# Kernel tuning notes

Hardware: AMD Instinct MI355X
Metric: run time of the kernel (lower is better)

Reference implementation:

```python
import jax, jax.numpy as jnp
import numpy as np

DIM, DEPTH, HEADS = 1024, 6, 16
B, N = 2, 1024
QB = 128.0   # 8-bit activation absmax quant: Qb = 2**(8-1)
EPS = 1e-5


def setup_inputs() -> dict:
    key = jax.random.key(0)
    ks = jax.random.split(key, 4)
    x = jax.random.normal(ks[0], (B, N, DIM), dtype=jnp.float32)
    # BitLinear weights (per layer, two per FFN block), latent fp weights
    ff_w1 = jax.random.normal(ks[1], (DEPTH, DIM, DIM), dtype=jnp.float32) * 0.02
    ff_w2 = jax.random.normal(ks[2], (DEPTH, DIM, DIM), dtype=jnp.float32) * 0.02
    # LayerNorm params (inside FeedForward) and final norm
    ff_ln_g = jnp.ones((DEPTH, DIM), jnp.float32)
    ff_ln_b = jnp.zeros((DEPTH, DIM), jnp.float32)
    final_ln_g = jnp.ones((DIM,), jnp.float32)
    final_ln_b = jnp.zeros((DIM,), jnp.float32)
    return dict(x=x, ff_ln_g=ff_ln_g, ff_ln_b=ff_ln_b, ff_w1=ff_w1,
                ff_w2=ff_w2, final_ln_g=final_ln_g, final_ln_b=final_ln_b)


def layernorm(x, g, b):
    m = jnp.mean(x, axis=-1, keepdims=True)
    v = jnp.mean((x - m) ** 2, axis=-1, keepdims=True)
    return (x - m) * jax.lax.rsqrt(v + EPS) * g + b


def bitlinear(x, w):
    # BitNet b1: binarize weights around their mean, absmax-quantize activations to 8 bits,
    # int-style matmul, then rescale by beta*gamma/Qb.
    alpha = jnp.mean(w)
    w_b = jnp.sign(w - alpha)                 # ternary/binary weights {-1,0,+1}
    beta = jnp.mean(jnp.abs(w))               # ||W||_1 / (n*m)
    gamma = jnp.max(jnp.abs(x))               # activation absmax
    x_q = jnp.clip(x * (QB / gamma), -QB + EPS, QB - EPS)
    y = jnp.einsum('...i,oi->...o', x_q, w_b)
    return y * (beta * gamma / QB)


def attend(x):
    # non-flash multi-head self-attention, q=k=v=x (Attend has no projections)
    b, n, d = x.shape
    dh = d // HEADS
    q = x.reshape(b, n, HEADS, dh).transpose(0, 2, 1, 3)          # bhnd
    scores = jnp.einsum('bhid,bhjd->bhij', q, q) * (dh ** -0.5)   # [B,H,N,N]
    attn = jax.nn.softmax(scores, axis=-1)
    out = jnp.einsum('bhij,bhjd->bhid', attn, q)
    return out.transpose(0, 2, 1, 3).reshape(b, n, d)


def reference(x, ff_ln_g, ff_ln_b, ff_w1, ff_w2, final_ln_g, final_ln_b):
    for i in range(DEPTH):
        x = attend(x) + x
        h = layernorm(x, ff_ln_g[i], ff_ln_b[i])
        h = bitlinear(h, ff_w1[i])
        h = jax.nn.gelu(h, approximate=False)   # torch nn.GELU default = exact
        h = bitlinear(h, ff_w2[i])
        x = h + x
    return layernorm(x, final_ln_g, final_ln_b)
```

## Files before the change

### kernel.cpp

```cpp
#include <hip/hip_runtime.h>
#include <math.h>

typedef __attribute__((ext_vector_type(4))) float f32x4;
typedef __attribute__((ext_vector_type(8))) _Float16 f16x8;

__device__ __forceinline__ f32x4 mfma16h(f16x8 a, f16x8 b, f32x4 c){
  return __builtin_amdgcn_mfma_f32_16x16x32_f16(a, b, c, 0, 0, 0);
}
__device__ __forceinline__ void gload_lds16(const void* g, void* l){
  __builtin_amdgcn_global_load_lds((const __attribute__((address_space(1))) void*)g,
                                   (__attribute__((address_space(3))) void*)l, 16, 0, 0);
}

#define EXPC 0.1803368801111204f

__global__ __launch_bounds__(256) void k_wstats(const float* __restrict__ w1, const float* __restrict__ w2,
                                                double* __restrict__ dsum, double* __restrict__ dabs){
  const int mat = blockIdx.y;
  const float* wp = (mat < 6) ? (w1 + (size_t)mat*1048576) : (w2 + (size_t)(mat-6)*1048576);
  const f32x4* wv = (const f32x4*)wp + (size_t)blockIdx.x*8192;
  double s = 0.0, a = 0.0;
  for (int j = 0; j < 32; j++){
    f32x4 v = wv[j*256 + threadIdx.x];
    s += (double)v.x + (double)v.y + (double)v.z + (double)v.w;
    a += (double)fabsf(v.x) + (double)fabsf(v.y) + (double)fabsf(v.z) + (double)fabsf(v.w);
  }
  for (int d = 1; d < 64; d <<= 1){ s += __shfl_xor(s, d); a += __shfl_xor(a, d); }
  __shared__ double red[8];
  const int w = threadIdx.x >> 6;
  if ((threadIdx.x & 63) == 0){ red[w*2] = s; red[w*2+1] = a; }
  __syncthreads();
  if (threadIdx.x == 0){
    double S = red[0]+red[2]+red[4]+red[6], A = red[1]+red[3]+red[5]+red[7];
    atomicAdd(&dsum[mat], S);
    atomicAdd(&dabs[mat], A);
  }
}

__global__ __launch_bounds__(256) void k_binarize(const float* __restrict__ w1, const float* __restrict__ w2,
                                                  const double* __restrict__ dsum, _Float16* __restrict__ wb){
  const int blk = blockIdx.x;
  const int mat = blk >> 9;
  const float alpha = (float)(dsum[mat] * (1.0/1048576.0));
  const float* wp = (mat < 6) ? (w1 + (size_t)mat*1048576) : (w2 + (size_t)(mat-6)*1048576);
  const size_t off = (size_t)(blk & 511)*2048 + (size_t)threadIdx.x*8;
  const int n = (int)(off >> 10), k = (int)(off & 1023);
  f32x4 v0 = *(const f32x4*)(wp + off), v1 = *(const f32x4*)(wp + off + 4);
  float vv[8] = {v0.x,v0.y,v0.z,v0.w,v1.x,v1.y,v1.z,v1.w};
  f16x8 pk;
  #pragma unroll
  for (int e = 0; e < 8; e++){
    float d = vv[e] - alpha;
    pk[e] = d > 0.f ? (_Float16)1.0f : (d < 0.f ? (_Float16)(-1.0f) : (_Float16)0.0f);
  }
  const size_t addr = (size_t)mat*1048576 + (size_t)n*1024 + (size_t)((k & ~63) + ((k & 63) ^ ((n&7)*8)));
  *(f16x8*)&wb[addr] = pk;
}

__global__ __launch_bounds__(256) void k_presplit(const float* __restrict__ x,
                                                  _Float16* __restrict__ Kh, _Float16* __restrict__ Kl,
                                                  _Float16* __restrict__ Vh, _Float16* __restrict__ Vl){
  __shared__ _Float16 lh[64*72], ll[64*72];
  const int t = blockIdx.x, bh = blockIdx.y, b = bh>>4, h = bh&15;
  const int n = threadIdx.x>>2, c0 = (threadIdx.x&3)*16;
  const float* src = x + (size_t)b*1048576 + (size_t)(t*64+n)*1024 + h*64 + c0;
  const size_t kbase = ((size_t)bh*1024 + t*64 + n)*64;
  const int sw = (n&7)*8;
  #pragma unroll
  for (int j = 0; j < 2; j++){
    f32x4 v0 = *(const f32x4*)(src + j*8);
    f32x4 v1 = *(const f32x4*)(src + j*8 + 4);
    float vv[8] = {v0.x,v0.y,v0.z,v0.w,v1.x,v1.y,v1.z,v1.w};
    f16x8 Hv, Lv;
    #pragma unroll
    for (int e = 0; e < 8; e++){
      _Float16 hh = (_Float16)vv[e];
      Hv[e] = hh; Lv[e] = (_Float16)(vv[e] - (float)hh);
      const int d = c0 + j*8 + e;
      lh[d*72 + n] = Hv[e]; ll[d*72 + n] = Lv[e];
    }
    const int db = c0 + j*8;
    *(f16x8*)&Kh[kbase + (db ^ sw)] = Hv;
    *(f16x8*)&Kl[kbase + (db ^ sw)] = Lv;
  }
  __syncthreads();
  const int d = threadIdx.x>>2, n0c = (threadIdx.x&3)*16;
  const size_t vbase = ((size_t)bh*64 + d)*1024 + t*64;
  const int sw2 = (d&7)*8;
  #pragma unroll
  for (int j = 0; j < 2; j++){
    f16x8 Hv, Lv;
    #pragma unroll
    for (int e = 0; e < 8; e++){
      Hv[e] = lh[d*72 + n0c + j*8 + e];
      Lv[e] = ll[d*72 + n0c + j*8 + e];
    }
    const int nb = n0c + j*8;
    *(f16x8*)&Vh[vbase + (nb ^ sw2)] = Hv;
    *(f16x8*)&Vl[vbase + (nb ^ sw2)] = Lv;
  }
}

__global__ __launch_bounds__(256) void k_attn(const _Float16* __restrict__ Kh, const _Float16* __restrict__ Kl,
                                              const _Float16* __restrict__ Vh, const _Float16* __restrict__ Vl,
                                              const float* __restrict__ xin, float* __restrict__ xout){
  __shared__ _Float16 smb[40960];
  _Float16* ps_h = smb + 32768;
  _Float16* ps_l = smb + 36864;
  const int tid = threadIdx.x, w = tid>>6, l = tid&63, g = l>>4, r16 = l&15;
  const int bh = blockIdx.x, qt = blockIdx.y, b = bh>>4, h = bh&15;
  const int swr = (r16&7)*8;
  const _Float16* Kbh = Kh + (size_t)bh*65536;
  const _Float16* Kbl = Kl + (size_t)bh*65536;

  #define ASTAGE(buf, t) { _Float16* Bp = smb + (buf)*16384;                                    \
    _Pragma("unroll")                                                                            \
    for (int j = 0; j < 2; j++){                                                                 \
      const int cb = (j*4 + w)*64; const int c = cb + l;                                         \
      gload_lds16(Kbh + (size_t)(t)*4096 + (size_t)c*8, Bp + cb*8);                              \
      gload_lds16(Kbl + (size_t)(t)*4096 + (size_t)c*8, Bp + 4096 + cb*8);                       \
      gload_lds16(Vh + ((size_t)bh*64 + (c>>3))*1024 + (t)*64 + (c&7)*8, Bp + 8192 + cb*8);      \
      gload_lds16(Vl + ((size_t)bh*64 + (c>>3))*1024 + (t)*64 + (c&7)*8, Bp + 12288 + cb*8);     \
    } }

  const _Float16* Qsh = Kbh + (size_t)qt*4096;
  const _Float16* Qsl = Kbl + (size_t)qt*4096;
  #pragma unroll
  for (int j = 0; j < 2; j++){
    const int cb = (j*4 + w)*64;
    gload_lds16(Qsh + (size_t)(cb + l)*8, ps_h + cb*8);
    gload_lds16(Qsl + (size_t)(cb + l)*8, ps_l + cb*8);
  }
  ASTAGE(0, 0);
  __syncthreads();
  const int qrow = w*16 + r16;
  const f16x8 aqh0 = *(const f16x8*)&ps_h[qrow*64 + ((g*8) ^ swr)];
  const f16x8 aqh1 = *(const f16x8*)&ps_h[qrow*64 + ((32 + g*8) ^ swr)];
  const f16x8 aql0 = *(const f16x8*)&ps_l[qrow*64 + ((g*8) ^ swr)];
  const f16x8 aql1 = *(const f16x8*)&ps_l[qrow*64 + ((32 + g*8) ^ swr)];
  __syncthreads();
  float mI[4], lI[4]; f32x4 acc[4];
  #pragma unroll
  for (int i = 0; i < 4; i++){ mI[i] = -1e30f; lI[i] = 0.f; acc[i] = (f32x4){0.f,0.f,0.f,0.f}; }

  for (int t = 0; t < 16; t++){
    if (t < 15) ASTAGE((t+1)&1, t+1);
    const _Float16* kt_h = smb + (t&1)*16384;
    const _Float16* kt_l = kt_h + 4096;
    const _Float16* vt_h = kt_h + 8192;
    const _Float16* vt_l = kt_h + 12288;
    f32x4 s[4];
    #pragma unroll
    for (int c = 0; c < 4; c++){
      const int rk = c*16 + r16;
      const f16x8 kh0 = *(const f16x8*)&kt_h[rk*64 + ((g*8) ^ swr)];
      const f16x8 kh1 = *(const f16x8*)&kt_h[rk*64 + ((32+g*8) ^ swr)];
      const f16x8 kl0 = *(const f16x8*)&kt_l[rk*64 + ((g*8) ^ swr)];
      const f16x8 kl1 = *(const f16x8*)&kt_l[rk*64 + ((32+g*8) ^ swr)];
      f32x4 z = (f32x4){0.f,0.f,0.f,0.f};
      z = mfma16h(aqh0, kh0, z);
      z = mfma16h(aqh1, kh1, z);
      z = mfma16h(aql0, kh0, z);
      z = mfma16h(aql1, kh1, z);
      z = mfma16h(aqh0, kl0, z);
      z = mfma16h(aqh1, kl1, z);
      s[c] = z;
    }
    float rmax[4], rsum[4], mnC[4];
    #pragma unroll
    for (int i = 0; i < 4; i++) rmax[i] = fmaxf(fmaxf(s[0][i],s[1][i]), fmaxf(s[2][i],s[3][i]));
    for (int d = 1; d < 16; d <<= 1)
      #pragma unroll
      for (int i = 0; i < 4; i++) rmax[i] = fmaxf(rmax[i], __shfl_xor(rmax[i], d));
    const float dmax = fmaxf(fmaxf(rmax[0]-mI[0], rmax[1]-mI[1]), fmaxf(rmax[2]-mI[2], rmax[3]-mI[3]));
    if (dmax > 44.36f){
      #pragma unroll
      for (int i = 0; i < 4; i++){
        const float mn = fmaxf(mI[i], rmax[i]);
        const float fac = exp2f((mI[i] - mn)*EXPC);
        lI[i] *= fac;
        mI[i] = mn;
        #pragma unroll
        for (int dc = 0; dc < 4; dc++) acc[dc][i] *= fac;
      }
    }
    #pragma unroll
    for (int i = 0; i < 4; i++){ mnC[i] = mI[i]*EXPC; rsum[i] = 0.f; }
    #pragma unroll
    for (int c = 0; c < 4; c++)
      #pragma unroll
      for (int i = 0; i < 4; i++){
        float p = exp2f(fmaf(s[c][i], EXPC, -mnC[i]));
        _Float16 ph = (_Float16)p;
        const int prow = w*16 + g*4 + i;
        const int pcol = (c*16 + r16) ^ ((2*g + (i>>1))*8);
        ps_h[prow*64 + pcol] = ph;
        ps_l[prow*64 + pcol] = (_Float16)(p - (float)ph);
        rsum[i] += p;
      }
    for (int d = 1; d < 16; d <<= 1)
      #pragma unroll
      for (int i = 0; i < 4; i++) rsum[i] += __shfl_xor(rsum[i], d);
    #pragma unroll
    for (int i = 0; i < 4; i++) lI[i] += rsum[i];
    const int psw = (r16>>1)*8;
    #pragma unroll
    for (int ks = 0; ks < 2; ks++){
      const f16x8 aph = *(const f16x8*)&ps_h[(w*16+r16)*64 + ((ks*32 + g*8) ^ psw)];
      const f16x8 apl = *(const f16x8*)&ps_l[(w*16+r16)*64 + ((ks*32 + g*8) ^ psw)];
      #pragma unroll
      for (int dc = 0; dc < 4; dc++){
        const int vr = dc*16 + r16;
        const f16x8 bvh = *(const f16x8*)&vt_h[vr*64 + ((ks*32 + g*8) ^ swr)];
        const f16x8 bvl = *(const f16x8*)&vt_l[vr*64 + ((ks*32 + g*8) ^ swr)];
        acc[dc] = mfma16h(aph, bvh, acc[dc]);
        acc[dc] = mfma16h(apl, bvh, acc[dc]);
        acc[dc] = mfma16h(aph, bvl, acc[dc]);
      }
    }
    __syncthreads();
  }
  #undef ASTAGE
  #pragma unroll
  for (int dc = 0; dc < 4; dc++)
    #pragma unroll
    for (int i = 0; i < 4; i++){
      const int row = qt*64 + w*16 + g*4 + i;
      const size_t idx = (size_t)b*1048576 + (size_t)row*1024 + h*64 + dc*16 + r16;
      xout[idx] = acc[dc][i]/lI[i] + xin[idx];
    }
}

template<int SPLIT>
__global__ __launch_bounds__(256) void k_ln(const float* __restrict__ x, const float* __restrict__ gg,
                                            const float* __restrict__ bb, float* __restrict__ outf,
                                            _Float16* __restrict__ Oh, _Float16* __restrict__ Ol){
  const int row = blockIdx.x*4 + (threadIdx.x>>6);
  const int lane = threadIdx.x & 63;
  const float* xr = x + (size_t)row*1024;
  f32x4 v[4];
  float s = 0.f, q = 0.f;
  #pragma unroll
  for (int c = 0; c < 2; c++){
    v[c*2]   = *(const f32x4*)(xr + c*512 + lane*8);
    v[c*2+1] = *(const f32x4*)(xr + c*512 + lane*8 + 4);
    #pragma unroll
    for (int e = 0; e < 4; e++){
      s += v[c*2][e] + v[c*2+1][e];
      q += v[c*2][e]*v[c*2][e] + v[c*2+1][e]*v[c*2+1][e];
    }
  }
  for (int d = 1; d < 64; d <<= 1){ s += __shfl_xor(s,d); q += __shfl_xor(q,d); }
  const float mean = s * (1.f/1024.f);
  const float var  = q * (1.f/1024.f) - mean*mean;
  const float rstd = rsqrtf(var + 1e-5f);
  #pragma unroll
  for (int c = 0; c < 2; c++){
    const int col = c*512 + lane*8;
    f32x4 g0 = *(const f32x4*)(gg + col), g1 = *(const f32x4*)(gg + col + 4);
    f32x4 b0 = *(const f32x4*)(bb + col), b1 = *(const f32x4*)(bb + col + 4);
    float h[8];
    #pragma unroll
    for (int e = 0; e < 4; e++){
      h[e]   = (v[c*2][e]  -mean)*rstd*g0[e] + b0[e];
      h[e+4] = (v[c*2+1][e]-mean)*rstd*g1[e] + b1[e];
    }
    if (SPLIT){
      f16x8 Hv, Lv;
      #pragma unroll
      for (int e = 0; e < 8; e++){
        _Float16 hh = (_Float16)h[e];
        Hv[e] = hh; Lv[e] = (_Float16)(h[e] - (float)hh);
      }
      const size_t addr = (size_t)row*1024 + c*512 + (lane>>3)*64 + (((lane&7)*8) ^ ((row&7)*8));
      *(f16x8*)&Oh[addr] = Hv;
      *(f16x8*)&Ol[addr] = Lv;
    } else {
      f32x4 o0, o1;
      #pragma unroll
      for (int e = 0; e < 4; e++){ o0[e] = h[e]; o1[e] = h[e+4]; }
      *(f32x4*)(outf + (size_t)row*1024 + col) = o0;
      *(f32x4*)(outf + (size_t)row*1024 + col + 4) = o1;
    }
  }
}

template<int MODE>
__global__ __launch_bounds__(256) void k_gemm(const _Float16* __restrict__ Ah, const _Float16* __restrict__ Al,
                                              const _Float16* __restrict__ Wg,
                                              float* __restrict__ out32,
                                              _Float16* __restrict__ Oh, _Float16* __restrict__ Ol,
                                              const double* __restrict__ dabs_slot){
  __shared__ _Float16 smb[24576];
  const int tid = threadIdx.x, w = tid>>6, l = tid&63, g = l>>4, r16 = l&15;
  const int wm = w>>1, wn = w&1;
  const int n0 = blockIdx.x*64, m0 = blockIdx.y*64;
  const float scale = (float)(*dabs_slot * (1.0/1048576.0));
  const int swr = (r16&7)*8;
  f32x4 acc[2][2] = {};
  #define STAGE(buf, k0) { _Float16* Bp = smb + (buf)*12288;                              \
    _Pragma("unroll")                                                                     \
    for (int j = 0; j < 2; j++){                                                          \
      const int cb = (j*4 + w)*64; const int c = cb + l;                                  \
      const int r = c>>3; const int cc = (c&7)*8;                                         \
      gload_lds16(Ah + (size_t)(m0 + r)*1024 + (k0) + cc, Bp + cb*8);                     \
      gload_lds16(Al + (size_t)(m0 + r)*1024 + (k0) + cc, Bp + 4096 + cb*8);              \
      gload_lds16(Wg + (size_t)(n0 + r)*1024 + (k0) + cc, Bp + 8192 + cb*8);              \
    } }
  STAGE(0, 0);
  __syncthreads();
  for (int t = 0; t < 16; t++){
    if (t < 15) STAGE((t+1)&1, (t+1)*64);
    const _Float16* Bp = smb + (t&1)*12288;
    #pragma unroll
    for (int kk = 0; kk < 2; kk++){
      f16x8 ah[2], al[2], bf[2];
      const int col = (kk*32 + g*8) ^ swr;
      #pragma unroll
      for (int mi = 0; mi < 2; mi++){
        const int row = wm*32 + mi*16 + r16;
        ah[mi] = *(const f16x8*)&Bp[row*64 + col];
        al[mi] = *(const f16x8*)&Bp[4096 + row*64 + col];
      }
      #pragma unroll
      for (int ni = 0; ni < 2; ni++){
        const int row = wn*32 + ni*16 + r16;
        bf[ni] = *(const f16x8*)&Bp[8192 + row*64 + col];
      }
      #pragma unroll
      for (int mi = 0; mi < 2; mi++)
        #pragma unroll
        for (int ni = 0; ni < 2; ni++){
          acc[mi][ni] = mfma16h(ah[mi], bf[ni], acc[mi][ni]);
          acc[mi][ni] = mfma16h(al[mi], bf[ni], acc[mi][ni]);
        }
    }
    __syncthreads();
  }
  #undef STAGE
  #pragma unroll
  for (int mi = 0; mi < 2; mi++)
    #pragma unroll
    for (int ni = 0; ni < 2; ni++)
      #pragma unroll
      for (int i = 0; i < 4; i++){
        const int rr = m0 + wm*32 + mi*16 + g*4 + i;
        const int cc = n0 + wn*32 + ni*16 + r16;
        float vv = acc[mi][ni][i] * scale;
        if (MODE == 0){
          vv = 0.5f*vv*(1.f + erff(vv*0.70710678118f));
          _Float16 hh = (_Float16)vv;
          const size_t addr = (size_t)rr*1024 + (cc & ~63) + ((cc & 63) ^ ((rr&7)*8));
          Oh[addr] = hh;
          Ol[addr] = (_Float16)(vv - (float)hh);
        } else {
          out32[(size_t)rr*1024 + cc] += vv;
        }
      }
}

extern "C" void kernel_launch(void* const* d_in, const int* in_sizes, int n_in,
                              void* d_out, int out_size, void* d_ws, size_t ws_size,
                              hipStream_t stream){
  const float* x_in = (const float*)d_in[0];
  const float* ln_g = (const float*)d_in[1];
  const float* ln_b = (const float*)d_in[2];
  const float* w1   = (const float*)d_in[3];
  const float* w2   = (const float*)d_in[4];
  const float* fg   = (const float*)d_in[5];
  const float* fb   = (const float*)d_in[6];

  char* ws = (char*)d_ws;
  double*   dsum  = (double*)ws;
  double*   dabs  = (double*)(ws + 96);
  _Float16* wb = (_Float16*)(ws + 256);
  size_t o = 256 + 12ull*1048576ull*2ull;
  float* xA = (float*)(ws + o); o += 2048ull*1024*4;
  float* xB = (float*)(ws + o); o += 2048ull*1024*4;
  _Float16* Kh = (_Float16*)(ws + o); o += 2048ull*1024*2;
  _Float16* Kl = (_Float16*)(ws + o); o += 2048ull*1024*2;
  _Float16* Vh = (_Float16*)(ws + o); o += 2048ull*1024*2;
  _Float16* Vl = (_Float16*)(ws + o); o += 2048ull*1024*2;
  _Float16* Ahb = (_Float16*)(ws + o); o += 2048ull*1024*2;
  _Float16* Alb = (_Float16*)(ws + o); o += 2048ull*1024*2;
  _Float16* Ghb = (_Float16*)(ws + o); o += 2048ull*1024*2;
  _Float16* Glb = (_Float16*)(ws + o); o += 2048ull*1024*2;

  hipMemsetAsync(ws, 0, 256, stream);
  k_wstats  <<<dim3(32,12), 256, 0, stream>>>(w1, w2, dsum, dabs);
  k_binarize<<<6144,        256, 0, stream>>>(w1, w2, dsum, wb);

  const float* xc = x_in;
  for (int i = 0; i < 6; i++){
    float* xn = (i & 1) ? xB : xA;
    k_presplit<<<dim3(16,32), 256, 0, stream>>>(xc, Kh, Kl, Vh, Vl);
    k_attn    <<<dim3(32,16), 256, 0, stream>>>(Kh, Kl, Vh, Vl, xc, xn);
    k_ln<1>   <<<512, 256, 0, stream>>>(xn, ln_g + (size_t)i*1024, ln_b + (size_t)i*1024,
                                        nullptr, Ahb, Alb);
    k_gemm<0> <<<dim3(16,32), 256, 0, stream>>>(Ahb, Alb, wb + (size_t)i*1048576,
                                                nullptr, Ghb, Glb, &dabs[i]);
    k_gemm<1> <<<dim3(16,32), 256, 0, stream>>>(Ghb, Glb, wb + (size_t)(6+i)*1048576,
                                                xn, nullptr, nullptr, &dabs[6+i]);
    xc = xn;
  }
  k_ln<0><<<512, 256, 0, stream>>>(xc, fg, fb, (float*)d_out, nullptr, nullptr);
}
```

Before: 596.3 us.

## Compute transposed S tile so P stays in registers, skipping LDS round-trip

Swaps the MFMA operands in the QK^T step so each lane holds one query row's scores across the key dimension. The P fragments can then be packed directly into registers as the A-operand of the PV MFMA, instead of being written to and read back from LDS. The K and Q swizzle and permutation are reworked to match the new fragment layout. Row max and sum reductions shrink to two cross-lane shuffles on a single scalar per lane, and the epilogue uses a reciprocal multiply. The new index permutations are intricate and a mistake would silently break correctness.

```diff
diff --git a/kernel.cpp b/kernel.cpp
--- a/kernel.cpp
+++ b/kernel.cpp
@@ -65,7 +65,7 @@
   const int n = threadIdx.x>>2, c0 = (threadIdx.x&3)*16;
   const float* src = x + (size_t)b*1048576 + (size_t)(t*64+n)*1024 + h*64 + c0;
   const size_t kbase = ((size_t)bh*1024 + t*64 + n)*64;
-  const int sw = (n&7)*8;
+  const int sw = ((((n>>4)&1)<<2) | (((n>>3)&1)<<1) | (n&1)) * 8;
   #pragma unroll
   for (int j = 0; j < 2; j++){
     f32x4 v0 = *(const f32x4*)(src + j*8);
@@ -105,43 +105,55 @@
                                               const _Float16* __restrict__ Vh, const _Float16* __restrict__ Vl,
                                               const float* __restrict__ xin, float* __restrict__ xout){
   __shared__ _Float16 smb[40960];
-  _Float16* ps_h = smb + 32768;
-  _Float16* ps_l = smb + 36864;
+  _Float16* qs_h = smb + 32768;
+  _Float16* qs_l = smb + 36864;
   const int tid = threadIdx.x, w = tid>>6, l = tid&63, g = l>>4, r16 = l&15;
   const int bh = blockIdx.x, qt = blockIdx.y, b = bh>>4, h = bh&15;
-  const int swr = (r16&7)*8;
   const _Float16* Kbh = Kh + (size_t)bh*65536;
   const _Float16* Kbl = Kl + (size_t)bh*65536;
 
-  #define ASTAGE(buf, t) { _Float16* Bp = smb + (buf)*16384;                                    \
-    _Pragma("unroll")                                                                            \
-    for (int j = 0; j < 2; j++){                                                                 \
-      const int cb = (j*4 + w)*64; const int c = cb + l;                                         \
-      gload_lds16(Kbh + (size_t)(t)*4096 + (size_t)c*8, Bp + cb*8);                              \
-      gload_lds16(Kbl + (size_t)(t)*4096 + (size_t)c*8, Bp + 4096 + cb*8);                       \
-      gload_lds16(Vh + ((size_t)bh*64 + (c>>3))*1024 + (t)*64 + (c&7)*8, Bp + 8192 + cb*8);      \
-      gload_lds16(Vl + ((size_t)bh*64 + (c>>3))*1024 + (t)*64 + (c&7)*8, Bp + 12288 + cb*8);     \
+  size_t koffK[2], voff[2];
+  int cbj[2];
+  #pragma unroll
+  for (int j = 0; j < 2; j++){
+    const int cb = (j*4 + w)*64, c = cb + l;
+    const int p  = c>>3;
+    const int kp = (p&32) | ((p&12)<<1) | ((p&16)>>2) | (p&3);
+    cbj[j]   = cb;
+    koffK[j] = (size_t)kp*64 + (size_t)(l&7)*8;
+    voff[j]  = ((size_t)bh*64 + (c>>3))*1024 + (size_t)(c&7)*8;
+  }
+  #define ASTAGE(buf, t) { _Float16* Bp = smb + (buf)*16384;                         \
+    _Pragma("unroll")                                                                 \
+    for (int j = 0; j < 2; j++){                                                      \
+      gload_lds16(Kbh + (size_t)(t)*4096 + koffK[j], Bp + cbj[j]*8);                  \
+      gload_lds16(Kbl + (size_t)(t)*4096 + koffK[j], Bp + 4096 + cbj[j]*8);           \
+      gload_lds16(Vh + voff[j] + (t)*64, Bp + 8192 + cbj[j]*8);                       \
+      gload_lds16(Vl + voff[j] + (t)*64, Bp + 12288 + cbj[j]*8);                      \
     } }
 
   const _Float16* Qsh = Kbh + (size_t)qt*4096;
   const _Float16* Qsl = Kbl + (size_t)qt*4096;
   #pragma unroll
   for (int j = 0; j < 2; j++){
-    const int cb = (j*4 + w)*64;
-    gload_lds16(Qsh + (size_t)(cb + l)*8, ps_h + cb*8);
-    gload_lds16(Qsl + (size_t)(cb + l)*8, ps_l + cb*8);
+    const int cb = cbj[j];
+    gload_lds16(Qsh + (size_t)(cb + l)*8, qs_h + cb*8);
+    gload_lds16(Qsl + (size_t)(cb + l)*8, qs_l + cb*8);
   }
   ASTAGE(0, 0);
   __syncthreads();
   const int qrow = w*16 + r16;
-  const f16x8 aqh0 = *(const f16x8*)&ps_h[qrow*64 + ((g*8) ^ swr)];
-  const f16x8 aqh1 = *(const f16x8*)&ps_h[qrow*64 + ((32 + g*8) ^ swr)];
-  const f16x8 aql0 = *(const f16x8*)&ps_l[qrow*64 + ((g*8) ^ swr)];
-  const f16x8 aql1 = *(const f16x8*)&ps_l[qrow*64 + ((32 + g*8) ^ swr)];
-  __syncthreads();
-  float mI[4], lI[4]; f32x4 acc[4];
-  #pragma unroll
-  for (int i = 0; i < 4; i++){ mI[i] = -1e30f; lI[i] = 0.f; acc[i] = (f32x4){0.f,0.f,0.f,0.f}; }
+  const int phq8 = (((w&1)<<2) | (((r16>>3)&1)<<1) | (r16&1)) * 8;
+  const int swk8 = ((((r16>>3)&1)<<2) | (((r16>>2)&1)<<1) | (r16&1)) * 8;
+  const int swr8 = (r16&7)*8;
+  const f16x8 aqh0 = *(const f16x8*)&qs_h[qrow*64 + ((g*8) ^ phq8)];
+  const f16x8 aqh1 = *(const f16x8*)&qs_h[qrow*64 + ((32 + g*8) ^ phq8)];
+  const f16x8 aql0 = *(const f16x8*)&qs_l[qrow*64 + ((g*8) ^ phq8)];
+  const f16x8 aql1 = *(const f16x8*)&qs_l[qrow*64 + ((32 + g*8) ^ phq8)];
+  float mI = -1e30f, lI = 0.f;
+  f32x4 acc[4];
+  #pragma unroll
+  for (int i = 0; i < 4; i++) acc[i] = (f32x4){0.f,0.f,0.f,0.f};
 
   for (int t = 0; t < 16; t++){
     if (t < 15) ASTAGE((t+1)&1, t+1);
@@ -153,82 +165,80 @@
     #pragma unroll
     for (int c = 0; c < 4; c++){
       const int rk = c*16 + r16;
-      const f16x8 kh0 = *(const f16x8*)&kt_h[rk*64 + ((g*8) ^ swr)];
-      const f16x8 kh1 = *(const f16x8*)&kt_h[rk*64 + ((32+g*8) ^ swr)];
-      const f16x8 kl0 = *(const f16x8*)&kt_l[rk*64 + ((g*8) ^ swr)];
-      const f16x8 kl1 = *(const f16x8*)&kt_l[rk*64 + ((32+g*8) ^ swr)];
+      const f16x8 kh0 = *(const f16x8*)&kt_h[rk*64 + ((g*8) ^ swk8)];
+      const f16x8 kh1 = *(const f16x8*)&kt_h[rk*64 + ((32+g*8) ^ swk8)];
+      const f16x8 kl0 = *(const f16x8*)&kt_l[rk*64 + ((g*8) ^ swk8)];
+      const f16x8 kl1 = *(const f16x8*)&kt_l[rk*64 + ((32+g*8) ^ swk8)];
       f32x4 z = (f32x4){0.f,0.f,0.f,0.f};
-      z = mfma16h(aqh0, kh0, z);
-      z = mfma16h(aqh1, kh1, z);
-      z = mfma16h(aql0, kh0, z);
-      z = mfma16h(aql1, kh1, z);
-      z = mfma16h(aqh0, kl0, z);
-      z = mfma16h(aqh1, kl1, z);
+      z = mfma16h(kh0, aqh0, z);
+      z = mfma16h(kh1, aqh1, z);
+      z = mfma16h(kh0, aql0, z);
+      z = mfma16h(kh1, aql1, z);
+      z = mfma16h(kl0, aqh0, z);
+      z = mfma16h(kl1, aqh1, z);
       s[c] = z;
     }
-    float rmax[4], rsum[4], mnC[4];
-    #pragma unroll
-    for (int i = 0; i < 4; i++) rmax[i] = fmaxf(fmaxf(s[0][i],s[1][i]), fmaxf(s[2][i],s[3][i]));
-    for (int d = 1; d < 16; d <<= 1)
-      #pragma unroll
-      for (int i = 0; i < 4; i++) rmax[i] = fmaxf(rmax[i], __shfl_xor(rmax[i], d));
-    const float dmax = fmaxf(fmaxf(rmax[0]-mI[0], rmax[1]-mI[1]), fmaxf(rmax[2]-mI[2], rmax[3]-mI[3]));
-    if (dmax > 44.36f){
+    float rmax = s[0][0];
+    #pragma unroll
+    for (int c = 0; c < 4; c++)
+      #pragma unroll
+      for (int i = 0; i < 4; i++) rmax = fmaxf(rmax, s[c][i]);
+    rmax = fmaxf(rmax, __shfl_xor(rmax, 16));
+    rmax = fmaxf(rmax, __shfl_xor(rmax, 32));
+    if (__any(rmax - mI > 44.36f)){
+      const float mn = fmaxf(mI, rmax);
+      const float fac = exp2f((mI - mn)*EXPC);
+      lI *= fac;
+      mI = mn;
       #pragma unroll
       for (int i = 0; i < 4; i++){
-        const float mn = fmaxf(mI[i], rmax[i]);
-        const float fac = exp2f((mI[i] - mn)*EXPC);
-        lI[i] *= fac;
-        mI[i] = mn;
+        const float fi = __shfl(fac, g*4 + i);
         #pragma unroll
-        for (int dc = 0; dc < 4; dc++) acc[dc][i] *= fac;
-      }
-    }
-    #pragma unroll
-    for (int i = 0; i < 4; i++){ mnC[i] = mI[i]*EXPC; rsum[i] = 0.f; }
+        for (int dc = 0; dc < 4; dc++) acc[dc][i] *= fi;
+      }
+    }
+    const float mC = mI*EXPC;
+    float rsum = 0.f;
+    f16x8 aph[2], apl[2];
     #pragma unroll
     for (int c = 0; c < 4; c++)
       #pragma unroll
       for (int i = 0; i < 4; i++){
-        float p = exp2f(fmaf(s[c][i], EXPC, -mnC[i]));
-        _Float16 ph = (_Float16)p;
-        const int prow = w*16 + g*4 + i;
-        const int pcol = (c*16 + r16) ^ ((2*g + (i>>1))*8);
-        ps_h[prow*64 + pcol] = ph;
-        ps_l[prow*64 + pcol] = (_Float16)(p - (float)ph);
-        rsum[i] += p;
-      }
-    for (int d = 1; d < 16; d <<= 1)
-      #pragma unroll
-      for (int i = 0; i < 4; i++) rsum[i] += __shfl_xor(rsum[i], d);
-    #pragma unroll
-    for (int i = 0; i < 4; i++) lI[i] += rsum[i];
-    const int psw = (r16>>1)*8;
+        const float p = exp2f(fmaf(s[c][i], EXPC, -mC));
+        const _Float16 ph = (_Float16)p;
+        aph[c>>1][(c&1)*4 + i] = ph;
+        apl[c>>1][(c&1)*4 + i] = (_Float16)(p - (float)ph);
+        rsum += p;
+      }
+    rsum += __shfl_xor(rsum, 16);
+    rsum += __shfl_xor(rsum, 32);
+    lI += rsum;
     #pragma unroll
     for (int ks = 0; ks < 2; ks++){
-      const f16x8 aph = *(const f16x8*)&ps_h[(w*16+r16)*64 + ((ks*32 + g*8) ^ psw)];
-      const f16x8 apl = *(const f16x8*)&ps_l[(w*16+r16)*64 + ((ks*32 + g*8) ^ psw)];
       #pragma unroll
       for (int dc = 0; dc < 4; dc++){
         const int vr = dc*16 + r16;
-        const f16x8 bvh = *(const f16x8*)&vt_h[vr*64 + ((ks*32 + g*8) ^ swr)];
-        const f16x8 bvl = *(const f16x8*)&vt_l[vr*64 + ((ks*32 + g*8) ^ swr)];
-        acc[dc] = mfma16h(aph, bvh, acc[dc]);
-        acc[dc] = mfma16h(apl, bvh, acc[dc]);
-        acc[dc] = mfma16h(aph, bvl, acc[dc]);
+        const f16x8 bvh = *(const f16x8*)&vt_h[vr*64 + ((ks*32 + g*8) ^ swr8)];
+        const f16x8 bvl = *(const f16x8*)&vt_l[vr*64 + ((ks*32 + g*8) ^ swr8)];
+        acc[dc] = mfma16h(aph[ks], bvh, acc[dc]);
+        acc[dc] = mfma16h(apl[ks], bvh, acc[dc]);
+        acc[dc] = mfma16h(aph[ks], bvl, acc[dc]);
       }
     }
     __syncthreads();
   }
   #undef ASTAGE
   #pragma unroll
-  for (int dc = 0; dc < 4; dc++)
-    #pragma unroll
-    for (int i = 0; i < 4; i++){
-      const int row = qt*64 + w*16 + g*4 + i;
+  for (int i = 0; i < 4; i++){
+    const float li = __shfl(lI, g*4 + i);
+    const float inv = 1.f/li;
+    const int row = qt*64 + w*16 + g*4 + i;
+    #pragma unroll
+    for (int dc = 0; dc < 4; dc++){
       const size_t idx = (size_t)b*1048576 + (size_t)row*1024 + h*64 + dc*16 + r16;
-      xout[idx] = acc[dc][i]/lI[i] + xin[idx];
-    }
+      xout[idx] = acc[dc][i]*inv + xin[idx];
+    }
+  }
 }
 
 template<int SPLIT>
```

After: 520.4 us. 12.7% less time.
